# Optimization experiments

Hardware: AMD Instinct MI355X
Metric: run time of the kernel (lower is better)

## Reference

```python
import jax, jax.numpy as jnp
import numpy as np

BATCH, LENGTH, DIM = 2, 2048, 1024
DIM_HIDDEN, NUM_HEAD = 1024, 8
BASE_LR, BASE_WD = 0.01, 0.01


def setup_inputs() -> dict:
    key = jax.random.key(0)
    ks = jax.random.split(key, 8)
    s = jnp.float32(0.02)  # init scale for linear weights
    f32 = jnp.float32
    return {
        "x": jax.random.normal(ks[0], (BATCH, LENGTH, DIM), f32),
        "hidden": jax.random.normal(ks[1], (BATCH, DIM, DIM_HIDDEN), f32),
        "log_base_lr": jnp.full((NUM_HEAD,), float(np.log(BASE_LR)), f32),
        "fc_lr_w": jax.random.normal(ks[2], (DIM, NUM_HEAD), f32) * s,
        "fc_lr_b": jnp.zeros((NUM_HEAD,), f32),
        "log_base_wd": jnp.full((NUM_HEAD,), float(np.log(BASE_WD)), f32),
        "fc_wd_w": jax.random.normal(ks[3], (DIM, NUM_HEAD), f32) * s,
        "fc_wd_b": jnp.zeros((NUM_HEAD,), f32),
        "wq": jax.random.normal(ks[4], (DIM, DIM_HIDDEN), f32) * s,
        "bq": jnp.zeros((DIM_HIDDEN,), f32),
        "wk": jax.random.normal(ks[5], (DIM, DIM_HIDDEN), f32) * s,
        "bk": jnp.zeros((DIM_HIDDEN,), f32),
        "wv": jax.random.normal(ks[6], (DIM, DIM), f32) * s,
        "bv": jnp.zeros((DIM,), f32),
    }


def reference(x, hidden, log_base_lr, fc_lr_w, fc_lr_b, log_base_wd, fc_wd_w, fc_wd_b, wq, bq, wk, bk, wv, bv):
    b, L, dim = x.shape
    n = log_base_lr.shape[0]
    dim_hidden = wq.shape[1]
    dh = dim_hidden // n

    W_prev = hidden.reshape(b, dim, n, dh).transpose(0, 2, 1, 3)          # [b,n,dim,h]
    q = (x @ wq + bq).reshape(b, L, n, dh).transpose(0, 2, 1, 3)          # [b,n,L,h]
    k = (x @ wk + bk).reshape(b, L, n, dh).transpose(0, 2, 1, 3)          # [b,n,L,h]
    v = x @ wv + bv                                                        # [b,L,dim]

    lr = (jnp.exp(log_base_lr) * jax.nn.sigmoid(x @ fc_lr_w + fc_lr_b)).transpose(0, 2, 1)   # [b,n,L]
    lwd = jnp.log1p(-jnp.exp(log_base_wd) * jax.nn.sigmoid(x @ fc_wd_w + fc_wd_b)).transpose(0, 2, 1)  # [b,n,L]

    wd_cross = jnp.exp(jnp.cumsum(lwd, axis=2))                            # [b,n,L]
    # einops.repeat 'b n l -> b n m l' then triu(1), cumsum over m, exp, triu
    rep = jnp.broadcast_to(lwd[:, :, None, :], (b, n, L, L))               # [b,n,m,l]
    wd_inner = jnp.triu(jnp.exp(jnp.cumsum(jnp.triu(rep, 1), axis=2)))     # [b,n,L,L]

    kq = jnp.einsum('bnld,bnmd->bnlm', k, q)                               # [b,n,L,L]
    mask_kq = kq * wd_inner

    WpK_V = jnp.einsum('bndh,bnlh->bnld', W_prev, k) - v[:, None]          # [b,n,L,dim]

    y_inner = -jnp.einsum('bnld,bnl,bnlm->bmd', WpK_V, lr, mask_kq)        # [b,L,dim]
    y_cross = jnp.einsum('bndh,bnlh,bnl->bld', W_prev, q, wd_cross)        # [b,L,dim]
    y = y_inner + y_cross

    Wn_inner = -jnp.einsum('bnld,bnl,bnlh->bndh', WpK_V, lr * wd_inner[:, :, :, -1], k)
    Wn_cross = W_prev * wd_cross[:, :, -1][:, :, None, None]
    W_next = (Wn_inner + Wn_cross).transpose(0, 2, 1, 3).reshape(b, dim, dim_hidden)
    return (y, W_next)
```

## Files before the change

### kernel.cpp

```cpp
#include <hip/hip_runtime.h>
#include <stdint.h>


typedef __bf16 bf16x8 __attribute__((ext_vector_type(8)));
typedef float f32x4 __attribute__((ext_vector_type(4)));
typedef unsigned short u16;
typedef u16 u16x4 __attribute__((ext_vector_type(4)));

#define MFMA16 __builtin_amdgcn_mfma_f32_16x16x32_bf16

static __device__ __forceinline__ u16 f2b(float f) {
  union { float f; uint32_t u; } v; v.f = f;
  uint32_t r = v.u + 0x7FFFu + ((v.u >> 16) & 1u);
  return (u16)(r >> 16);
}
static __device__ __forceinline__ float b2f(u16 h) {
  union { uint32_t u; float f; } v; v.u = ((uint32_t)h) << 16;
  return v.f;
}

typedef __attribute__((address_space(1))) void gvoid_t;
typedef __attribute__((address_space(3))) void lvoid_t;
static __device__ __forceinline__ void gld16(const u16* g, u16* l) {
  __builtin_amdgcn_global_load_lds((gvoid_t*)(uintptr_t)g, (lvoid_t*)l, 16, 0, 0);
}

static __device__ __forceinline__ void stage64(u16* lds, const u16* __restrict__ g, int ld, int t) {
  const int r0 = t >> 2, c0 = (t & 3) << 3;
  const u16* ga = g + (size_t)r0 * ld + c0;
  const u16* gb = g + (size_t)(r0 + 64) * ld + c0;
  u16* la = lds + (r0 << 5) + c0;
  u16* lb = lds + ((r0 + 64) << 5) + c0;
  gld16(ga, la);
  gld16(gb, lb);
  gld16(ga + 32, la + 4096);
  gld16(gb + 32, lb + 4096);
}

#define TILE_IDS                                   \
  const int t = threadIdx.x;                       \
  const int w = t >> 6, ln = t & 63;               \
  const int wr = (w >> 1) << 6, wc = (w & 1) << 6; \
  const int q = ln >> 4, q8 = q << 3, r = ln & 15;

static __device__ __forceinline__ void mfma_tile64(const u16* As, const u16* Bs,
                                                   int wr, int wc, int q8, int r, f32x4 acc[4][4]) {
#pragma unroll
  for (int kk = 0; kk < 2; ++kk) {
    const u16* Ak = As + (kk << 12);
    const u16* Bk = Bs + (kk << 12);
    bf16x8 af[4], bf[4];
#pragma unroll
    for (int s = 0; s < 4; ++s) af[s] = *(const bf16x8*)(Ak + ((wr + s * 16 + r) << 5) + q8);
#pragma unroll
    for (int s = 0; s < 4; ++s) bf[s] = *(const bf16x8*)(Bk + ((wc + s * 16 + r) << 5) + q8);
#pragma unroll
    for (int sm = 0; sm < 4; ++sm)
#pragma unroll
      for (int sn = 0; sn < 4; ++sn)
        acc[sm][sn] = MFMA16(af[sm], bf[sn], acc[sm][sn], 0, 0, 0);
  }
}

static __device__ __forceinline__ void gemm_loop(u16* As, u16* Bs,
    const u16* __restrict__ A, int lda, const u16* __restrict__ B, int ldb, int nc,
    int wr, int wc, int q8, int r, int t, f32x4 acc[4][4]) {
  for (int c = 0; c < nc; ++c) {
    __syncthreads();
    stage64(As, A + c * 64, lda, t);
    stage64(Bs, B + c * 64, ldb, t);
    __syncthreads();
    mfma_tile64(As, Bs, wr, wc, q8, r, acc);
  }
}


__global__ __launch_bounds__(256) void k_prep(const float* __restrict__ x,
    const float* __restrict__ hidden, const float* __restrict__ wq,
    const float* __restrict__ wk, const float* __restrict__ wv,
    const float* __restrict__ wlr, const float* __restrict__ blr,
    const float* __restrict__ wwd, const float* __restrict__ bwd,
    const float* __restrict__ lbl, const float* __restrict__ lbw,
    u16* __restrict__ xb, u16* __restrict__ hb, u16* __restrict__ wqT,
    u16* __restrict__ wkT, u16* __restrict__ wvT,
    float* __restrict__ lr, float* __restrict__ lwd) {
  __shared__ float smem[4352];
  const int bid = blockIdx.x, t = threadIdx.x;
  if (bid < 4096) {
    const size_t i = ((size_t)bid * 256 + t) * 4;
    f32x4 v = *(const f32x4*)(x + i);
    u16x4 o;
#pragma unroll
    for (int j = 0; j < 4; ++j) o[j] = f2b(v[j]);
    *(u16x4*)(xb + i) = o;
  } else if (bid < 6144) {
    const size_t i = ((size_t)(bid - 4096) * 256 + t) * 4;
    f32x4 v = *(const f32x4*)(hidden + i);
    u16x4 o;
#pragma unroll
    for (int j = 0; j < 4; ++j) o[j] = f2b(v[j]);
    *(u16x4*)(hb + i) = o;
  } else if (bid < 9216) {
    const int idx = bid - 6144;
    const int z = idx >> 10, rem = idx & 1023;
    const float* src = z == 0 ? wq : z == 1 ? wk : wv;
    u16* dst = z == 0 ? wqT : z == 1 ? wkT : wvT;
    const int k0 = (rem >> 5) * 32, n0 = (rem & 31) * 32;
    float (*tile)[33] = (float(*)[33])smem;
    const int tx = t & 31, ty = t >> 5;
#pragma unroll
    for (int i = 0; i < 4; ++i)
      tile[ty + i * 8][tx] = src[(size_t)(k0 + ty + i * 8) * 1024 + n0 + tx];
    __syncthreads();
#pragma unroll
    for (int i = 0; i < 4; ++i)
      dst[(size_t)(n0 + ty + i * 8) * 1024 + k0 + tx] = f2b(tile[tx][ty + i * 8]);
  } else {
    const int row = bid - 9216;
    float pl[8] = {}, pw[8] = {};
    const float* xr = x + (size_t)row * 1024;
    for (int i = t; i < 1024; i += 256) {
      const float xv = xr[i];
      const float* wl = wlr + (size_t)i * 8;
      const float* ww = wwd + (size_t)i * 8;
#pragma unroll
      for (int j = 0; j < 8; ++j) { pl[j] += xv * wl[j]; pw[j] += xv * ww[j]; }
    }
    float (*red)[17] = (float(*)[17])smem;
#pragma unroll
    for (int j = 0; j < 8; ++j) { red[t][j] = pl[j]; red[t][j + 8] = pw[j]; }
    __syncthreads();
    for (int s = 128; s > 0; s >>= 1) {
      if (t < s) {
#pragma unroll
        for (int j = 0; j < 16; ++j) red[t][j] += red[t + s][j];
      }
      __syncthreads();
    }
    const int b = row >> 11, l = row & 2047;
    if (t < 8) {
      const float sig = 1.f / (1.f + expf(-(red[0][t] + blr[t])));
      lr[((size_t)b * 8 + t) * 2048 + l] = expf(lbl[t]) * sig;
    } else if (t < 16) {
      const int j = t - 8;
      const float sig = 1.f / (1.f + expf(-(red[0][t] + bwd[j])));
      lwd[((size_t)b * 8 + j) * 2048 + l] = log1pf(-expf(lbw[j]) * sig);
    }
  }
}


__global__ __launch_bounds__(256) void k_scan(const float* __restrict__ lwd,
                                              float* __restrict__ wdc, float* __restrict__ wdlast) {
  const int bn = blockIdx.x, t = threadIdx.x;
  const float* src = lwd + (size_t)bn * 2048;
  float v[8], s = 0.f;
#pragma unroll
  for (int i = 0; i < 8; ++i) { v[i] = src[t * 8 + i]; s += v[i]; }
  __shared__ float ps[256];
  ps[t] = s;
  __syncthreads();
  for (int off = 1; off < 256; off <<= 1) {
    const float add = (t >= off) ? ps[t - off] : 0.f;
    __syncthreads();
    ps[t] += add;
    __syncthreads();
  }
  float run = ps[t] - s;
  const float lwd_last = src[2047];
  float* wo = wdc + (size_t)bn * 2048;
  float* wl = wdlast + (size_t)bn * 2048;
#pragma unroll
  for (int i = 0; i < 8; ++i) {
    run += v[i];
    const int idx = t * 8 + i;
    wo[idx] = expf(run);
    const int c = (idx + 1 < 2047) ? (idx + 1) : 2047;
    wl[idx] = expf(lwd_last * (float)c);
  }
}


__global__ __launch_bounds__(256) void k_qkv(const u16* __restrict__ xb,
    const u16* __restrict__ wqT, const u16* __restrict__ wkT, const u16* __restrict__ wvT,
    const float* __restrict__ bq, const float* __restrict__ bk, const float* __restrict__ bv,
    const float* __restrict__ wdl,
    u16* __restrict__ qb, u16* __restrict__ kb, u16* __restrict__ vT, u16* __restrict__ kTw) {
  __shared__ u16 As[8192], Bs[8192];
  TILE_IDS
  const int bid = blockIdx.x;
  f32x4 acc[4][4] = {};
  if (bid < 512) {
    const int z = bid >> 8, rem = bid & 255;
    const int m0 = (rem >> 3) * 128, n0 = (rem & 7) * 128;
    gemm_loop(As, Bs, xb + (size_t)m0 * 1024, 1024,
              (z ? wkT : wqT) + (size_t)n0 * 1024, 1024, 16, wr, wc, q8, r, t, acc);
    const float* bias = z ? bk : bq;
    u16* outp = z ? kb : qb;
#pragma unroll
    for (int sn = 0; sn < 4; ++sn) {
      const int col = n0 + wc + sn * 16 + r;
      const float bc = bias[col];
#pragma unroll
      for (int sm = 0; sm < 4; ++sm)
#pragma unroll
        for (int i = 0; i < 4; ++i) {
          const int gm = m0 + wr + sm * 16 + (q << 2) + i;
          outp[(size_t)gm * 1024 + col] = f2b(acc[sm][sn][i] + bc);
        }
    }
  } else {
    const int idx = bid - 512;
    const int zz = idx >> 7, rem = idx & 127;
    const int sel = zz >> 1, b = zz & 1;
    const int m0 = (rem >> 4) * 128, l0 = (rem & 15) * 128;
    gemm_loop(As, Bs, (sel ? wkT : wvT) + (size_t)m0 * 1024, 1024,
              xb + ((size_t)(b * 2048 + l0)) * 1024, 1024, 16, wr, wc, q8, r, t, acc);
#pragma unroll
    for (int sm = 0; sm < 4; ++sm)
#pragma unroll
      for (int i = 0; i < 4; ++i) {
        const int row = m0 + wr + sm * 16 + (q << 2) + i;
        const float bc = sel ? bk[row] : bv[row];
#pragma unroll
        for (int sn = 0; sn < 4; ++sn) {
          const int l = l0 + wc + sn * 16 + r;
          const float v = acc[sm][sn][i] + bc;
          if (!sel) {
            vT[((size_t)(b * 1024 + row)) * 2048 + l] = f2b(v);
          } else {
            const int n = row >> 7;
            kTw[((size_t)(b * 1024 + row)) * 2048 + l] =
                f2b(v * wdl[((size_t)(b * 8 + n)) * 2048 + l]);
          }
        }
      }
  }
}


__global__ __launch_bounds__(256) void k_mid(const u16* __restrict__ qb,
    const u16* __restrict__ kb, const u16* __restrict__ hb, const u16* __restrict__ vT,
    const float* __restrict__ lr, const float* __restrict__ lwd, const float* __restrict__ wdc,
    const float* __restrict__ hidden,
    u16* __restrict__ S, u16* __restrict__ AfT, float* __restrict__ y, float* __restrict__ out2) {
  __shared__ u16 As[8192], Bs[8192];
  TILE_IDS
  const int bid = blockIdx.x;
  if (bid < 2176) {
    const int p = bid % 136, bn = bid / 136, b = bn >> 3, n = bn & 7;
    int mi = (int)((sqrtf(8.f * p + 1.f) - 1.f) * 0.5f);
    while ((mi + 1) * (mi + 2) / 2 <= p) ++mi;
    while (mi * (mi + 1) / 2 > p) --mi;
    const int li = p - mi * (mi + 1) / 2;
    const int m0 = mi * 128, l0 = li * 128;
    f32x4 acc[4][4] = {};
    gemm_loop(As, Bs, qb + ((size_t)(b * 2048 + m0)) * 1024 + n * 128, 1024,
              kb + ((size_t)(b * 2048 + l0)) * 1024 + n * 128, 1024, 2, wr, wc, q8, r, t, acc);
    const float* lwdp = lwd + (size_t)bn * 2048;
    u16* Sp = S + (size_t)bn * 2048 * 2048;
#pragma unroll
    for (int sm = 0; sm < 4; ++sm)
#pragma unroll
      for (int i = 0; i < 4; ++i) {
        const int m = m0 + wr + sm * 16 + (q << 2) + i;
        const float lm = lwdp[m];
#pragma unroll
        for (int sn = 0; sn < 4; ++sn) {
          const int l = l0 + wc + sn * 16 + r;
          float v = 0.f;
          if (l <= m) {
            const float c = (l == m) ? (float)m : (float)(l + 1);
            v = -acc[sm][sn][i] * __expf(lm * c);
          }
          Sp[(size_t)m * 2048 + l] = f2b(v);
        }
      }
  } else if (bid < 4224) {
    const int idx = bid - 2176;
    const int bn = idx >> 7, rem = idx & 127;
    const int l0 = (rem >> 3) * 128, d0 = (rem & 7) * 128;
    const int b = bn >> 3, n = bn & 7;
    f32x4 acc[4][4] = {};
    gemm_loop(As, Bs, hb + ((size_t)(b * 1024 + d0)) * 1024 + n * 128, 1024,
              kb + ((size_t)(b * 2048 + l0)) * 1024 + n * 128, 1024, 2, wr, wc, q8, r, t, acc);
    const float* lrp = lr + (size_t)bn * 2048;
#pragma unroll
    for (int sm = 0; sm < 4; ++sm)
#pragma unroll
      for (int i = 0; i < 4; ++i) {
        const int d = d0 + wr + sm * 16 + (q << 2) + i;
#pragma unroll
        for (int sn = 0; sn < 4; ++sn) {
          const int l = l0 + wc + sn * 16 + r;
          const float v = (acc[sm][sn][i] - b2f(vT[((size_t)(b * 1024 + d)) * 2048 + l])) * lrp[l];
          AfT[((size_t)bn * 1024 + d) * 2048 + l] = f2b(v);
        }
      }
  } else if (bid < 5248) {
    const size_t i = ((size_t)(bid - 4224) * 256 + t) * 16;
#pragma unroll
    for (int j = 0; j < 4; ++j)
      *(f32x4*)(y + i + j * 4) = f32x4{0.f, 0.f, 0.f, 0.f};
  } else {
    const size_t i = ((size_t)(bid - 5248) * 256 + t) * 4;
    const int b = (int)(i >> 20);
    const int hd = (int)(i & 1023);
    const float wdcl = wdc[((size_t)(b * 8 + (hd >> 7))) * 2048 + 2047];
    f32x4 v = *(const f32x4*)(hidden + i);
    v *= wdcl;
    *(f32x4*)(out2 + i) = v;
  }
}


__global__ __launch_bounds__(256) void k_qs(u16* __restrict__ qb, const float* __restrict__ wdc) {
  const size_t base = ((size_t)blockIdx.x * 256 + threadIdx.x) * 4;
  const int b = (int)(base >> 21);
  const int rem = (int)(base & 2097151);
  const int m = rem >> 10, hd = rem & 1023;
  const float sc = wdc[((size_t)b * 8 + (hd >> 7)) * 2048 + m];
  u16x4 v = *(const u16x4*)(qb + base);
#pragma unroll
  for (int j = 0; j < 4; ++j) v[j] = f2b(b2f(v[j]) * sc);
  *(u16x4*)(qb + base) = v;
}


__global__ __launch_bounds__(256) void k_fin(const u16* __restrict__ S,
    const u16* __restrict__ AfT, const u16* __restrict__ Qs, const u16* __restrict__ hb,
    const u16* __restrict__ kTw, float* __restrict__ y, float* __restrict__ out2) {
  __shared__ u16 As[8192], Bs[8192];
  TILE_IDS
  const int bid = blockIdx.x;
  if (bid < 1024) {
    const int z = bid >> 6, rem = bid & 63;
    const int mip = rem >> 3, dj = rem & 7;
    const int b = z >> 3, n = z & 7;
    const int d0 = dj * 128;
    float* Y = y + (size_t)b * 2048 * 1024;
#pragma unroll 1
    for (int tsel = 0; tsel < 2; ++tsel) {
      const int mi = tsel ? (15 - mip) : mip;
      const int m0 = mi * 128;
      f32x4 acc[4][4] = {};
      gemm_loop(As, Bs, S + (size_t)z * 2048 * 2048 + (size_t)m0 * 2048, 2048,
                AfT + ((size_t)z * 1024 + d0) * 2048, 2048, 2 * mi + 2, wr, wc, q8, r, t, acc);
      gemm_loop(As, Bs, Qs + ((size_t)(b * 2048 + m0)) * 1024 + n * 128, 1024,
                hb + ((size_t)(b * 1024 + d0)) * 1024 + n * 128, 1024, 2, wr, wc, q8, r, t, acc);
#pragma unroll
      for (int sm = 0; sm < 4; ++sm)
#pragma unroll
        for (int i = 0; i < 4; ++i) {
          const int m = m0 + wr + sm * 16 + (q << 2) + i;
#pragma unroll
          for (int sn = 0; sn < 4; ++sn)
            atomicAdd(&Y[(size_t)m * 1024 + d0 + wc + sn * 16 + r], acc[sm][sn][i]);
        }
    }
  } else {
    const int idx = bid - 1024;
    const int z = idx >> 6, rem = idx & 63;
    const int d0 = (rem >> 3) * 128, nj = rem & 7;
    const int b = z >> 2, kc = z & 3;
    const int bn = b * 8 + nj;
    f32x4 acc[4][4] = {};
    gemm_loop(As, Bs, AfT + ((size_t)bn * 1024 + d0) * 2048 + kc * 512, 2048,
              kTw + ((size_t)(b * 1024 + nj * 128)) * 2048 + kc * 512, 2048, 8,
              wr, wc, q8, r, t, acc);
#pragma unroll
    for (int sm = 0; sm < 4; ++sm)
#pragma unroll
      for (int i = 0; i < 4; ++i) {
        const int d = d0 + wr + sm * 16 + (q << 2) + i;
#pragma unroll
        for (int sn = 0; sn < 4; ++sn) {
          const int hd = nj * 128 + wc + sn * 16 + r;
          atomicAdd(&out2[((size_t)(b * 1024 + d)) * 1024 + hd], -acc[sm][sn][i]);
        }
      }
  }
}


extern "C" void kernel_launch(void* const* d_in, const int* in_sizes, int n_in,
                              void* d_out, int out_size, void* d_ws, size_t ws_size,
                              hipStream_t stream) {
  const float* x      = (const float*)d_in[0];
  const float* hidden = (const float*)d_in[1];
  const float* lbl    = (const float*)d_in[2];
  const float* wlr    = (const float*)d_in[3];
  const float* blr    = (const float*)d_in[4];
  const float* lbw    = (const float*)d_in[5];
  const float* wwd    = (const float*)d_in[6];
  const float* bwd    = (const float*)d_in[7];
  const float* wq     = (const float*)d_in[8];
  const float* bq     = (const float*)d_in[9];
  const float* wk     = (const float*)d_in[10];
  const float* bk     = (const float*)d_in[11];
  const float* wv     = (const float*)d_in[12];
  const float* bv     = (const float*)d_in[13];
  float* out = (float*)d_out;

  char* ws = (char*)d_ws;
  const size_t MB = 1u << 20;
  u16* S     = (u16*)(ws);
  u16* xb    = (u16*)(ws);
  u16* wqT   = (u16*)(ws + 8 * MB);
  u16* wkT   = (u16*)(ws + 10 * MB);
  u16* wvT   = (u16*)(ws + 12 * MB);
  u16* AfT   = (u16*)(ws + 128 * MB);
  u16* hb    = (u16*)(ws + 192 * MB);
  u16* qb    = (u16*)(ws + 196 * MB);
  u16* kb    = (u16*)(ws + 204 * MB);
  u16* kTw   = (u16*)(ws + 212 * MB);
  u16* vT    = (u16*)(ws + 220 * MB);
  float* lr  = (float*)(ws + 228 * MB);
  float* lwd = (float*)(ws + 228 * MB + 131072);
  float* wdc = (float*)(ws + 228 * MB + 262144);
  float* wdl = (float*)(ws + 228 * MB + 393216);
  (void)ws_size; (void)n_in; (void)in_sizes; (void)out_size;

  const size_t YSZ = (size_t)2 * 2048 * 1024;

  k_prep<<<13312, 256, 0, stream>>>(x, hidden, wq, wk, wv, wlr, blr, wwd, bwd,
                                    lbl, lbw, xb, hb, wqT, wkT, wvT, lr, lwd);
  k_scan<<<16, 256, 0, stream>>>(lwd, wdc, wdl);
  k_qkv<<<1024, 256, 0, stream>>>(xb, wqT, wkT, wvT, bq, bk, bv, wdl, qb, kb, vT, kTw);
  k_mid<<<7296, 256, 0, stream>>>(qb, kb, hb, vT, lr, lwd, wdc, hidden, S, AfT, out, out + YSZ);
  k_qs<<<4096, 256, 0, stream>>>(qb, wdc);
  k_fin<<<1536, 256, 0, stream>>>(S, AfT, qb, hb, kTw, out, out + YSZ);
}
```

Baseline: 431.0 us.

## Enlarge k_fin output tiles to 128x256 with 512-thread blocks

Result: slower. 448.7 us (+4.1%).

```diff
diff --git a/kernel.cpp b/kernel.cpp
--- a/kernel.cpp
+++ b/kernel.cpp
@@ -37,18 +37,37 @@
   gld16(gb + 32, lb + 4096);
 }
 
+static __device__ __forceinline__ void stage128_T512(u16* lds, const u16* __restrict__ g,
+                                                     int ld, int t) {
+  const int r0 = t >> 2, c0 = (t & 3) << 3;
+  const u16* ga = g + (size_t)r0 * ld + c0;
+  gld16(ga, lds + t * 8);
+  gld16(ga + 32, lds + 4096 + t * 8);
+}
+static __device__ __forceinline__ void stage256_T512(u16* lds, const u16* __restrict__ g,
+                                                     int ld, int t) {
+#pragma unroll
+  for (int j = 0; j < 2; ++j) {
+    const int i = j * 512 + t;
+    const int r0 = i >> 2, c0 = (i & 3) << 3;
+    const u16* ga = g + (size_t)r0 * ld + c0;
+    gld16(ga, lds + i * 8);
+    gld16(ga + 32, lds + 8192 + i * 8);
+  }
+}
+
 #define TILE_IDS                                   \
   const int t = threadIdx.x;                       \
   const int w = t >> 6, ln = t & 63;               \
   const int wr = (w >> 1) << 6, wc = (w & 1) << 6; \
   const int q = ln >> 4, q8 = q << 3, r = ln & 15;
 
-static __device__ __forceinline__ void mfma_tile64(const u16* As, const u16* Bs,
-                                                   int wr, int wc, int q8, int r, f32x4 acc[4][4]) {
+static __device__ __forceinline__ void mfma64(const u16* As, const u16* Bs, int astr, int bstr,
+                                              int wr, int wc, int q8, int r, f32x4 acc[4][4]) {
 #pragma unroll
   for (int kk = 0; kk < 2; ++kk) {
-    const u16* Ak = As + (kk << 12);
-    const u16* Bk = Bs + (kk << 12);
+    const u16* Ak = As + kk * astr;
+    const u16* Bk = Bs + kk * bstr;
     bf16x8 af[4], bf[4];
 #pragma unroll
     for (int s = 0; s < 4; ++s) af[s] = *(const bf16x8*)(Ak + ((wr + s * 16 + r) << 5) + q8);
@@ -70,7 +89,7 @@
     stage64(As, A + c * 64, lda, t);
     stage64(Bs, B + c * 64, ldb, t);
     __syncthreads();
-    mfma_tile64(As, Bs, wr, wc, q8, r, acc);
+    mfma64(As, Bs, 4096, 4096, wr, wc, q8, r, acc);
   }
 }
 
@@ -327,27 +346,46 @@
 }
 
 
-__global__ __launch_bounds__(256) void k_fin(const u16* __restrict__ S,
+__global__ __launch_bounds__(512) void k_fin(const u16* __restrict__ S,
     const u16* __restrict__ AfT, const u16* __restrict__ Qs, const u16* __restrict__ hb,
     const u16* __restrict__ kTw, float* __restrict__ y, float* __restrict__ out2) {
-  __shared__ u16 As[8192], Bs[8192];
-  TILE_IDS
+  __shared__ u16 buf[24576];
+  const int t = threadIdx.x;
+  const int w = t >> 6, ln = t & 63;
+  const int q = ln >> 4, q8 = q << 3, r = ln & 15;
   const int bid = blockIdx.x;
-  if (bid < 1024) {
-    const int z = bid >> 6, rem = bid & 63;
-    const int mip = rem >> 3, dj = rem & 7;
+  if (bid < 512) {
+    u16* As = buf;
+    u16* Bs = buf + 8192;
+    const int z = bid >> 5, mip = (bid >> 2) & 7, dj = bid & 3;
     const int b = z >> 3, n = z & 7;
-    const int d0 = dj * 128;
+    const int d0 = dj * 256;
+    const int wr = (w >> 2) << 6, wc = (w & 3) << 6;
     float* Y = y + (size_t)b * 2048 * 1024;
 #pragma unroll 1
     for (int tsel = 0; tsel < 2; ++tsel) {
       const int mi = tsel ? (15 - mip) : mip;
       const int m0 = mi * 128;
       f32x4 acc[4][4] = {};
-      gemm_loop(As, Bs, S + (size_t)z * 2048 * 2048 + (size_t)m0 * 2048, 2048,
-                AfT + ((size_t)z * 1024 + d0) * 2048, 2048, 2 * mi + 2, wr, wc, q8, r, t, acc);
-      gemm_loop(As, Bs, Qs + ((size_t)(b * 2048 + m0)) * 1024 + n * 128, 1024,
-                hb + ((size_t)(b * 1024 + d0)) * 1024 + n * 128, 1024, 2, wr, wc, q8, r, t, acc);
+      const u16* A = S + (size_t)z * 2048 * 2048 + (size_t)m0 * 2048;
+      const u16* B = AfT + ((size_t)z * 1024 + d0) * 2048;
+      const int nc = 2 * mi + 2;
+      for (int c = 0; c < nc; ++c) {
+        __syncthreads();
+        stage128_T512(As, A + c * 64, 2048, t);
+        stage256_T512(Bs, B + c * 64, 2048, t);
+        __syncthreads();
+        mfma64(As, Bs, 4096, 8192, wr, wc, q8, r, acc);
+      }
+      const u16* A2 = Qs + ((size_t)(b * 2048 + m0)) * 1024 + n * 128;
+      const u16* B2 = hb + ((size_t)(b * 1024 + d0)) * 1024 + n * 128;
+      for (int c = 0; c < 2; ++c) {
+        __syncthreads();
+        stage128_T512(As, A2 + c * 64, 1024, t);
+        stage256_T512(Bs, B2 + c * 64, 1024, t);
+        __syncthreads();
+        mfma64(As, Bs, 4096, 8192, wr, wc, q8, r, acc);
+      }
 #pragma unroll
       for (int sm = 0; sm < 4; ++sm)
 #pragma unroll
@@ -359,15 +397,23 @@
         }
     }
   } else {
-    const int idx = bid - 1024;
-    const int z = idx >> 6, rem = idx & 63;
-    const int d0 = (rem >> 3) * 128, nj = rem & 7;
-    const int b = z >> 2, kc = z & 3;
+    u16* As = buf;
+    u16* Bs = buf + 16384;
+    const int idx = bid - 512;
+    const int di = idx >> 5, nj = (idx >> 2) & 7, b = (idx >> 1) & 1, kc = idx & 1;
+    const int d0 = di * 256;
     const int bn = b * 8 + nj;
+    const int wr = (w >> 1) << 6, wc = (w & 1) << 6;
     f32x4 acc[4][4] = {};
-    gemm_loop(As, Bs, AfT + ((size_t)bn * 1024 + d0) * 2048 + kc * 512, 2048,
-              kTw + ((size_t)(b * 1024 + nj * 128)) * 2048 + kc * 512, 2048, 8,
-              wr, wc, q8, r, t, acc);
+    const u16* A = AfT + ((size_t)bn * 1024 + d0) * 2048 + kc * 1024;
+    const u16* B = kTw + ((size_t)(b * 1024 + nj * 128)) * 2048 + kc * 1024;
+    for (int c = 0; c < 16; ++c) {
+      __syncthreads();
+      stage256_T512(As, A + c * 64, 2048, t);
+      stage128_T512(Bs, B + c * 64, 2048, t);
+      __syncthreads();
+      mfma64(As, Bs, 8192, 4096, wr, wc, q8, r, acc);
+    }
 #pragma unroll
     for (int sm = 0; sm < 4; ++sm)
 #pragma unroll
@@ -429,5 +475,5 @@
   k_qkv<<<1024, 256, 0, stream>>>(xb, wqT, wkT, wvT, bq, bk, bv, wdl, qb, kb, vT, kTw);
   k_mid<<<7296, 256, 0, stream>>>(qb, kb, hb, vT, lr, lwd, wdc, hidden, S, AfT, out, out + YSZ);
   k_qs<<<4096, 256, 0, stream>>>(qb, wdc);
-  k_fin<<<1536, 256, 0, stream>>>(S, AfT, qb, hb, kTw, out, out + YSZ);
-}
+  k_fin<<<640, 512, 0, stream>>>(S, AfT, qb, hb, kTw, out, out + YSZ);
+}
```

## Fold q decay scaling into QKV epilogue and compensate in S mask

Applied to the files above, without the earlier changes.

Measured after the change: 427.6 us. No clear change (-0.8%).

```diff
diff --git a/kernel.cpp b/kernel.cpp
--- a/kernel.cpp
+++ b/kernel.cpp
@@ -151,7 +151,7 @@
 
 
 __global__ __launch_bounds__(256) void k_scan(const float* __restrict__ lwd,
-                                              float* __restrict__ wdc, float* __restrict__ wdlast) {
+                                              float* __restrict__ cum, float* __restrict__ wdlast) {
   const int bn = blockIdx.x, t = threadIdx.x;
   const float* src = lwd + (size_t)bn * 2048;
   float v[8], s = 0.f;
@@ -168,13 +168,13 @@
   }
   float run = ps[t] - s;
   const float lwd_last = src[2047];
-  float* wo = wdc + (size_t)bn * 2048;
+  float* co = cum + (size_t)bn * 2048;
   float* wl = wdlast + (size_t)bn * 2048;
 #pragma unroll
   for (int i = 0; i < 8; ++i) {
     run += v[i];
     const int idx = t * 8 + i;
-    wo[idx] = expf(run);
+    co[idx] = run;
     const int c = (idx + 1 < 2047) ? (idx + 1) : 2047;
     wl[idx] = expf(lwd_last * (float)c);
   }
@@ -184,7 +184,7 @@
 __global__ __launch_bounds__(256) void k_qkv(const u16* __restrict__ xb,
     const u16* __restrict__ wqT, const u16* __restrict__ wkT, const u16* __restrict__ wvT,
     const float* __restrict__ bq, const float* __restrict__ bk, const float* __restrict__ bv,
-    const float* __restrict__ wdl,
+    const float* __restrict__ wdl, const float* __restrict__ cum,
     u16* __restrict__ qb, u16* __restrict__ kb, u16* __restrict__ vT, u16* __restrict__ kTw) {
   __shared__ u16 As[8192], Bs[8192];
   TILE_IDS
@@ -201,12 +201,18 @@
     for (int sn = 0; sn < 4; ++sn) {
       const int col = n0 + wc + sn * 16 + r;
       const float bc = bias[col];
+      const int n = col >> 7;
 #pragma unroll
       for (int sm = 0; sm < 4; ++sm)
 #pragma unroll
         for (int i = 0; i < 4; ++i) {
           const int gm = m0 + wr + sm * 16 + (q << 2) + i;
-          outp[(size_t)gm * 1024 + col] = f2b(acc[sm][sn][i] + bc);
+          float v = acc[sm][sn][i] + bc;
+          if (z == 0) {
+            const int b = gm >> 11, m = gm & 2047;
+            v *= __expf(cum[((size_t)(b * 8 + n)) * 2048 + m]);
+          }
+          outp[(size_t)gm * 1024 + col] = f2b(v);
         }
     }
   } else {
@@ -241,7 +247,7 @@
 
 __global__ __launch_bounds__(256) void k_mid(const u16* __restrict__ qb,
     const u16* __restrict__ kb, const u16* __restrict__ hb, const u16* __restrict__ vT,
-    const float* __restrict__ lr, const float* __restrict__ lwd, const float* __restrict__ wdc,
+    const float* __restrict__ lr, const float* __restrict__ lwd, const float* __restrict__ cum,
     const float* __restrict__ hidden,
     u16* __restrict__ S, u16* __restrict__ AfT, float* __restrict__ y, float* __restrict__ out2) {
   __shared__ u16 As[8192], Bs[8192];
@@ -258,6 +264,7 @@
     gemm_loop(As, Bs, qb + ((size_t)(b * 2048 + m0)) * 1024 + n * 128, 1024,
               kb + ((size_t)(b * 2048 + l0)) * 1024 + n * 128, 1024, 2, wr, wc, q8, r, t, acc);
     const float* lwdp = lwd + (size_t)bn * 2048;
+    const float* cump = cum + (size_t)bn * 2048;
     u16* Sp = S + (size_t)bn * 2048 * 2048;
 #pragma unroll
     for (int sm = 0; sm < 4; ++sm)
@@ -265,13 +272,14 @@
       for (int i = 0; i < 4; ++i) {
         const int m = m0 + wr + sm * 16 + (q << 2) + i;
         const float lm = lwdp[m];
+        const float cm = cump[m];
 #pragma unroll
         for (int sn = 0; sn < 4; ++sn) {
           const int l = l0 + wc + sn * 16 + r;
           float v = 0.f;
           if (l <= m) {
             const float c = (l == m) ? (float)m : (float)(l + 1);
-            v = -acc[sm][sn][i] * __expf(lm * c);
+            v = -acc[sm][sn][i] * __expf(lm * c - cm);
           }
           Sp[(size_t)m * 2048 + l] = f2b(v);
         }
@@ -306,24 +314,11 @@
     const size_t i = ((size_t)(bid - 5248) * 256 + t) * 4;
     const int b = (int)(i >> 20);
     const int hd = (int)(i & 1023);
-    const float wdcl = wdc[((size_t)(b * 8 + (hd >> 7))) * 2048 + 2047];
+    const float wdcl = __expf(cum[((size_t)(b * 8 + (hd >> 7))) * 2048 + 2047]);
     f32x4 v = *(const f32x4*)(hidden + i);
     v *= wdcl;
     *(f32x4*)(out2 + i) = v;
   }
-}
-
-
-__global__ __launch_bounds__(256) void k_qs(u16* __restrict__ qb, const float* __restrict__ wdc) {
-  const size_t base = ((size_t)blockIdx.x * 256 + threadIdx.x) * 4;
-  const int b = (int)(base >> 21);
-  const int rem = (int)(base & 2097151);
-  const int m = rem >> 10, hd = rem & 1023;
-  const float sc = wdc[((size_t)b * 8 + (hd >> 7)) * 2048 + m];
-  u16x4 v = *(const u16x4*)(qb + base);
-#pragma unroll
-  for (int j = 0; j < 4; ++j) v[j] = f2b(b2f(v[j]) * sc);
-  *(u16x4*)(qb + base) = v;
 }
 
 
@@ -334,8 +329,10 @@
   TILE_IDS
   const int bid = blockIdx.x;
   if (bid < 1024) {
-    const int z = bid >> 6, rem = bid & 63;
-    const int mip = rem >> 3, dj = rem & 7;
+    const int window = bid >> 6, within = bid & 63;
+    const int dj = within >> 3, low = within & 7;
+    const int g = window * 8 + low;
+    const int z = g >> 3, mip = g & 7;
     const int b = z >> 3, n = z & 7;
     const int d0 = dj * 128;
     float* Y = y + (size_t)b * 2048 * 1024;
@@ -417,7 +414,7 @@
   u16* vT    = (u16*)(ws + 220 * MB);
   float* lr  = (float*)(ws + 228 * MB);
   float* lwd = (float*)(ws + 228 * MB + 131072);
-  float* wdc = (float*)(ws + 228 * MB + 262144);
+  float* cum = (float*)(ws + 228 * MB + 262144);
   float* wdl = (float*)(ws + 228 * MB + 393216);
   (void)ws_size; (void)n_in; (void)in_sizes; (void)out_size;
 
@@ -425,9 +422,8 @@
 
   k_prep<<<13312, 256, 0, stream>>>(x, hidden, wq, wk, wv, wlr, blr, wwd, bwd,
                                     lbl, lbw, xb, hb, wqT, wkT, wvT, lr, lwd);
-  k_scan<<<16, 256, 0, stream>>>(lwd, wdc, wdl);
-  k_qkv<<<1024, 256, 0, stream>>>(xb, wqT, wkT, wvT, bq, bk, bv, wdl, qb, kb, vT, kTw);
-  k_mid<<<7296, 256, 0, stream>>>(qb, kb, hb, vT, lr, lwd, wdc, hidden, S, AfT, out, out + YSZ);
-  k_qs<<<4096, 256, 0, stream>>>(qb, wdc);
+  k_scan<<<16, 256, 0, stream>>>(lwd, cum, wdl);
+  k_qkv<<<1024, 256, 0, stream>>>(xb, wqT, wkT, wvT, bq, bk, bv, wdl, cum, qb, kb, vT, kTw);
+  k_mid<<<7296, 256, 0, stream>>>(qb, kb, hb, vT, lr, lwd, cum, hidden, S, AfT, out, out + YSZ);
   k_fin<<<1536, 256, 0, stream>>>(S, AfT, qb, hb, kTw, out, out + YSZ);
 }
```
